# Performance work log

Measured on AMD Instinct MI355X. Metric: run time of the kernel, lower is better.

The kernel has to match this reference:

```python
import jax, jax.numpy as jnp
import numpy as np
from jax import lax

TIME_DIM = 100   # time_feat_dim
MEM_DIM = 172    # node_feat_dim == memory_dim
TAU = 0.3        # energy_threshold
LAM = 0.01       # softshrink sparsity_threshold


def _layer_norm(x, w, b, eps=1e-5):
    m = x.mean(-1, keepdims=True)
    v = ((x - m) ** 2).mean(-1, keepdims=True)
    return (x - m) / jnp.sqrt(v + eps) * w + b


def _time_encode(t):
    # TGN time encoder: cos(t * 1/10^linspace(0,9,D)), fixed (non-trainable)
    freqs = 1.0 / (10.0 ** jnp.linspace(0.0, 9.0, TIME_DIM))
    return jnp.cos(t[..., None] * freqs)


def _softshrink(x, lam=LAM):
    return jnp.where(x > lam, x - lam, jnp.where(x < -lam, x + lam, 0.0))


def setup_inputs() -> dict:
    key = jax.random.key(0)
    ks = jax.random.split(key, 12)
    B, N, NUM_NODES = 8192, 32, 500000
    s = 0.02  # scale used by Global_Local_Filtering
    return {
        "node_ids": jnp.arange(B, dtype=jnp.int32),
        "neighbor_node_ids": jax.random.randint(ks[0], (B, N), 0, NUM_NODES, dtype=jnp.int32),
        "node_interact_times": jax.random.uniform(ks[1], (B,), dtype=jnp.float32) * 1000.0,
        "neighbor_times": jax.random.uniform(ks[2], (B, N), dtype=jnp.float32) * 1000.0,
        "node_memories": jnp.zeros((NUM_NODES, MEM_DIM), jnp.float32),
        "r1": s * jax.random.normal(ks[3], (TIME_DIM, MEM_DIM), jnp.float32),
        "i1": s * jax.random.normal(ks[4], (TIME_DIM, MEM_DIM), jnp.float32),
        "rb1": s * jax.random.normal(ks[5], (MEM_DIM,), jnp.float32),
        "ib1": s * jax.random.normal(ks[6], (MEM_DIM,), jnp.float32),
        "conv_w": 0.02 * jax.random.normal(ks[7], (MEM_DIM, MEM_DIM, 8), jnp.float32),
        "conv_b": 0.02 * jax.random.normal(ks[8], (MEM_DIM,), jnp.float32),
        "rhythm_w": 0.1 * jax.random.normal(ks[9], (272, 1, 4), jnp.float32),
        "lin_w": 0.05 * jax.random.normal(ks[10], (272, MEM_DIM), jnp.float32),
        "lin_b": 0.02 * jax.random.normal(ks[11], (MEM_DIM,), jnp.float32),
        "mb_ln_w": jnp.ones((MEM_DIM,), jnp.float32),
        "mb_ln_b": jnp.zeros((MEM_DIM,), jnp.float32),
        "ln_w": jnp.ones((MEM_DIM,), jnp.float32),
        "ln_b": jnp.zeros((MEM_DIM,), jnp.float32),
    }


def reference(node_ids, neighbor_node_ids, node_interact_times, neighbor_times,
              node_memories, r1, i1, rb1, ib1, conv_w, conv_b,
              rhythm_w, lin_w, lin_b, mb_ln_w, mb_ln_b, ln_w, ln_b):
    # ---- RhythmMemoryUpdater.update_memory ----
    messages = _time_encode(node_interact_times)                 # [B,100]
    old_mem = node_memories[node_ids]                            # [B,172] gather
    x = jnp.concatenate([messages, old_mem], axis=-1)[:, :, None]  # [B,272,1] (NCH)
    # depthwise Conv1d(272,272,k=4,pad=2,groups=272,no bias): length 1 -> 2
    x = lax.conv_general_dilated(x, rhythm_w, (1,), [(2, 2)],
                                 dimension_numbers=("NCH", "OIH", "NCH"),
                                 feature_group_count=272)        # [B,272,2]
    x = jnp.einsum("bcl,cd->bld", x, lin_w) + lin_b              # [B,2,172]
    new_mem = x.mean(axis=1)                                     # mean(dim=1) since 2 != memory_dim
    # set_memories: layer_norm then scatter; then gather + SeqFilter layernorm
    updated = node_memories.at[node_ids].set(_layer_norm(new_mem, mb_ln_w, mb_ln_b))
    gathered = lax.stop_gradient(updated[node_ids])              # memory bank is non-trainable (no_grad)
    root_node_time = _layer_norm(gathered, ln_w, ln_b)           # [B,172]

    # ---- neighbor branch: FSTS (Global_Local_Filtering + Conv1d) ----
    dt = node_interact_times[:, None] - neighbor_times           # [B,N]
    tfeat = _time_encode(dt)                                     # [B,N,100]
    tfeat = jnp.where((neighbor_node_ids == 0)[..., None], 0.0, tfeat)

    xf = jnp.fft.fft(tfeat, axis=1, norm="ortho")                # [B,N,100] complex
    energy = jnp.sum(jnp.abs(xf) ** 2, axis=-1)                  # [B,N]
    mask = (energy / (energy.mean() + 1e-6) >= TAU).astype(tfeat.dtype)
    low = xf * mask[..., None]
    o_r = jnp.einsum("bnc,cd->bnd", low.real, r1) - jnp.einsum("bnc,cd->bnd", low.imag, i1) + rb1
    o_i = jnp.einsum("bnc,cd->bnd", low.imag, r1) + jnp.einsum("bnc,cd->bnd", low.real, i1) + ib1
    y_fft = _softshrink(jax.nn.relu(o_r)) + 1j * _softshrink(jax.nn.relu(o_i))
    y = jnp.fft.ifft(y_fft, axis=1, norm="ortho").real           # [B,N,172]

    # Local_Correlation: Conv1d(172,172,k=8,pad=4) over neighbor axis, then mean over length
    yc = lax.conv_general_dilated(y.transpose(0, 2, 1), conv_w, (1,), [(4, 4)],
                                  dimension_numbers=("NCH", "OIH", "NCH"))
    yc = yc + conv_b[None, :, None]                              # [B,172,33]
    neighbor_out = yc.mean(axis=-1)                              # [B,172]

    return root_node_time + neighbor_out
```

## Files before the change

### kernel.cpp

```cpp
#include <hip/hip_runtime.h>
#include <hip/hip_bf16.h>
#include <math.h>

#define B_ 8192
#define NN 32
#define TD 100
#define MD 172
#define KD 1376
#define TAUC 0.3f
#define LAMC 0.01f

typedef __attribute__((ext_vector_type(8))) short short8;
typedef __attribute__((ext_vector_type(4))) float f32x4;

#define WS_U_OFF    256
#define U_BYTES     ((size_t)B_ * KD * 2)
#define CONVB_ELEMS (11 * 43 * 64 * 8)
#define WBIG_ELEMS  (22 * 7 * 64 * 8)
#define CS_ELEMS    (2 * 64 * 8)
#define ROOT_ELEMS  (11 * 9 * 64 * 8)

__device__ __forceinline__ float wred(float v) {
#pragma unroll
  for (int o = 32; o > 0; o >>= 1) v += __shfl_down(v, o, 64);
  return v;
}

__device__ __forceinline__ short bf16_bits(float f) {
  __hip_bfloat16 h = __float2bfloat16(f);
  return *(short*)&h;
}

__device__ __forceinline__ unsigned pack2(float a, float b) {
  return (unsigned)(unsigned short)bf16_bits(a) |
         ((unsigned)(unsigned short)bf16_bits(b) << 16);
}

__global__ __launch_bounds__(256) void k_mean(const int* __restrict__ nid,
                                              const float* __restrict__ t,
                                              const float* __restrict__ nt,
                                              float* __restrict__ ws) {
  __shared__ float fr[TD];
  __shared__ float part[4];
  int tid = threadIdx.x;
  if (tid < TD) fr[tid] = (float)exp(-9.0 * (double)tid / 99.0 * 2.302585092994045684);
  __syncthreads();
  int idx = blockIdx.x * 256 + tid;
  int b = idx >> 5;
  float s = 0.f;
  if (nid[idx] != 0) {
    float dt = t[b] - nt[idx];
    for (int c = 0; c < TD; ++c) { float v = cosf(dt * fr[c]); s = fmaf(v, v, s); }
  }
  s = wred(s);
  if ((tid & 63) == 0) part[tid >> 6] = s;
  __syncthreads();
  if (tid == 0) atomicAdd(ws, part[0] + part[1] + part[2] + part[3]);
}

__global__ __launch_bounds__(256) void k_prep(const float* __restrict__ conv_w,
                                              short* __restrict__ Bfrag) {
  int idx = blockIdx.x * 256 + threadIdx.x;
  if (idx >= CONVB_ELEMS) return;
  int j = idx & 7;
  int l = (idx >> 3) & 63;
  int s = (idx >> 9) % 43;
  int n0 = idx / (43 * 64 * 8);
  int k = s * 32 + (l >> 4) * 8 + j;
  int col = n0 * 16 + (l & 15);
  float v = (col < MD) ? conv_w[(long)col * KD + k] : 0.f;
  Bfrag[idx] = bf16_bits(v);
}

__global__ __launch_bounds__(256) void k_prep3(const float* __restrict__ r1,
                                               const float* __restrict__ i1,
                                               const float* __restrict__ rhythm_w,
                                               const float* __restrict__ lin_w,
                                               short* __restrict__ Wfrag,
                                               short* __restrict__ CSfrag,
                                               short* __restrict__ Rfrag) {
  int idx = blockIdx.x * 256 + threadIdx.x;
  const float inv_s = 0.17677669529663687f;
  if (idx < WBIG_ELEMS) {
    int j = idx & 7;
    int l = (idx >> 3) & 63;
    int s = (idx % 3584) >> 9;
    int n0 = idx / 3584;
    int k = s * 32 + (l >> 4) * 8 + j;
    int col = n0 * 16 + (l & 15);
    float v = 0.f;
    if (k < 200) {
      if (n0 < 11) {
        int d = col;
        if (d < MD) v = (k < 100) ? r1[k * MD + d] : -i1[(k - 100) * MD + d];
      } else {
        int d = col - 176;
        if (d >= 0 && d < MD) v = (k < 100) ? i1[k * MD + d] : r1[(k - 100) * MD + d];
      }
    }
    Wfrag[idx] = bf16_bits(v);
  } else if (idx < WBIG_ELEMS + CS_ELEMS) {
    int idx2 = idx - WBIG_ELEMS;
    int j = idx2 & 7;
    int l = (idx2 >> 3) & 63;
    int s = idx2 >> 9;
    int row = l & 15;
    int kq = s * 32 + (l >> 4) * 8 + j;
    float v = 0.f;
    if (row < 8) {
      int kp = (kq < 32) ? kq : kq - 32;
      int lo = row - 4; if (lo < 0) lo = 0;
      int hi = row + 28; if (hi > 31) hi = 31;
      double cs = 0.0, ss = 0.0;
      for (int n = lo; n <= hi; ++n) {
        double ang = 0.19634954084936207740 * (double)((kp * n) & 31);
        cs += cos(ang); ss += sin(ang);
      }
      v = ((kq < 32) ? (float)cs : -(float)ss) * inv_s;
    }
    CSfrag[idx2] = bf16_bits(v);
  } else if (idx < WBIG_ELEMS + CS_ELEMS + ROOT_ELEMS) {
    int idx4 = idx - WBIG_ELEMS - CS_ELEMS;
    int n = idx4 / 4608;
    int rem = idx4 % 4608;
    int s = rem >> 9;
    int l = (rem >> 3) & 63;
    int j = rem & 7;
    int k = s * 32 + (l >> 4) * 8 + j;
    int col = n * 16 + (l & 15);
    float v = 0.f;
    if (k < 272 && col < MD) {
      float hw = 0.5f * (rhythm_w[k * 4 + 1] + rhythm_w[k * 4 + 2]);
      v = hw * lin_w[k * MD + col];
    }
    Rfrag[idx4] = bf16_bits(v);
  }
}

__global__ __launch_bounds__(384, 8) void k_main(
    const int* __restrict__ nbr_id, const float* __restrict__ t,
    const float* __restrict__ nt, const float* __restrict__ rb1,
    const float* __restrict__ ib1, const float* __restrict__ ws0,
    const short* __restrict__ Wfrag, const short* __restrict__ CSfrag,
    short* __restrict__ u_out) {
  __shared__ __align__(16) short sA[32 * 232];
  __shared__ __align__(16) unsigned char s_un[12800];
  __shared__ float s_fr[TD];
  __shared__ float s_c32[32], s_s32[32], s_dt[32], s_z[32];
  __shared__ float s_energy[32];

  float* tf = (float*)s_un;
  short* Y = (short*)s_un;
  const int tid = threadIdx.x;
  const int b = blockIdx.x;
  const int l = tid & 63, w = tid >> 6;
  const float inv_s = 0.17677669529663687f;

  if (tid < 32) {
    double ang = 0.19634954084936207740 * (double)tid;
    s_c32[tid] = (float)cos(ang);
    s_s32[tid] = (float)sin(ang);
    int gi = b * NN + tid;
    int id = nbr_id[gi];
    float d = t[b] - nt[gi];
    s_z[tid]  = (id == 0) ? 0.f : 1.f;
    s_dt[tid] = (id == 0) ? 0.f : d;
    s_energy[tid] = 0.f;
  }
  if (tid < TD) s_fr[tid] = (float)exp(-9.0 * (double)tid / 99.0 * 2.302585092994045684);
  __syncthreads();

  for (int idx = tid; idx < NN * TD; idx += 384) {
    int n = idx / TD, c = idx - n * TD;
    tf[idx] = s_z[n] * cosf(s_dt[n] * s_fr[c]);
  }
  if (tid < 256) {
    int row = tid >> 3, q = tid & 7;
    *(uint2*)(sA + row * 232 + 200 + q * 4) = make_uint2(0u, 0u);
  }
  __syncthreads();

  for (int task = tid; task < 17 * 25; task += 384) {
    int k = task / 25, c4 = (task - k * 25) * 4;
    float ar0=0,ar1=0,ar2=0,ar3=0, ai0=0,ai1=0,ai2=0,ai3=0;
    for (int n = 0; n < NN; ++n) {
      float4 a = *(const float4*)(tf + n * TD + c4);
      int j = (k * n) & 31;
      float cw = s_c32[j], sw = s_s32[j];
      ar0 = fmaf(a.x, cw, ar0); ai0 = fmaf(a.x, -sw, ai0);
      ar1 = fmaf(a.y, cw, ar1); ai1 = fmaf(a.y, -sw, ai1);
      ar2 = fmaf(a.z, cw, ar2); ai2 = fmaf(a.z, -sw, ai2);
      ar3 = fmaf(a.w, cw, ar3); ai3 = fmaf(a.w, -sw, ai3);
    }
    ar0*=inv_s; ar1*=inv_s; ar2*=inv_s; ar3*=inv_s;
    ai0*=inv_s; ai1*=inv_s; ai2*=inv_s; ai3*=inv_s;
    float e = ar0*ar0+ar1*ar1+ar2*ar2+ar3*ar3 + ai0*ai0+ai1*ai1+ai2*ai2+ai3*ai3;
    atomicAdd(&s_energy[k], e);
    uint2 vr = make_uint2(pack2(ar0, ar1), pack2(ar2, ar3));
    uint2 vi = make_uint2(pack2(ai0, ai1), pack2(ai2, ai3));
    *(uint2*)(sA + k * 232 + c4) = vr;
    *(uint2*)(sA + k * 232 + 100 + c4) = vi;
    if (k >= 1 && k <= 15) {
      uint2 vin = make_uint2(pack2(-ai0, -ai1), pack2(-ai2, -ai3));
      *(uint2*)(sA + (32 - k) * 232 + c4) = vr;
      *(uint2*)(sA + (32 - k) * 232 + 100 + c4) = vin;
    }
  }
  __syncthreads();

  {
    float gth = TAUC * (ws0[0] * (1.0f / 262144.0f) + 1e-6f);
    for (int idx = tid; idx < 800; idx += 384) {
      int row = idx / 25, q = idx - row * 25;
      int ks = (row <= 16) ? row : 32 - row;
      if (s_energy[ks] < gth)
        *(uint4*)((char*)sA + row * 464 + q * 16) = make_uint4(0u,0u,0u,0u);
    }
  }
  __syncthreads();

  const int mside = (w >= 3) ? 1 : 0;
  const int wn = w % 3;
  short8 afrag[7];
  {
    const short* ab = sA + (mside * 16 + (l & 15)) * 232 + ((l >> 4) << 3);
#pragma unroll
    for (int s = 0; s < 7; ++s) afrag[s] = *(const short8*)(ab + s * 32);
  }
  for (int n = wn; n < 11; n += 3) {
    f32x4 acc = (f32x4)(0.f);
#pragma unroll
    for (int s = 0; s < 7; ++s) {
      short8 bb = *(const short8*)(Wfrag + (((n * 7 + s) * 64) + l) * 8);
      acc = __builtin_amdgcn_mfma_f32_16x16x32_bf16(afrag[s], bb, acc, 0, 0, 0);
    }
    int d = n * 16 + (l & 15);
    bool valid = (d < MD);
    float bias = valid ? rb1[d] : 0.f;
    float y0 = valid ? fmaxf(acc[0] + bias - LAMC, 0.f) : 0.f;
    float y1 = valid ? fmaxf(acc[1] + bias - LAMC, 0.f) : 0.f;
    float y2 = valid ? fmaxf(acc[2] + bias - LAMC, 0.f) : 0.f;
    float y3 = valid ? fmaxf(acc[3] + bias - LAMC, 0.f) : 0.f;
    *(uint2*)(Y + d * 32 + mside * 16 + ((l >> 4) << 2)) =
        make_uint2(pack2(y0, y1), pack2(y2, y3));
  }
  __syncthreads();

  f32x4 uacc[2];
  uacc[0] = (f32x4)(0.f); uacc[1] = (f32x4)(0.f);
  {
    short8 cs0 = *(const short8*)(CSfrag + (l << 3));
#pragma unroll
    for (int ti = 0; ti < 2; ++ti) {
      int nu = w + 6 * ti;
      if (nu < 11) {
        short8 bfr = *(const short8*)(Y + (nu * 16 + (l & 15)) * 32 + ((l >> 4) << 3));
        uacc[ti] = __builtin_amdgcn_mfma_f32_16x16x32_bf16(cs0, bfr, uacc[ti], 0, 0, 0);
      }
    }
  }
  __syncthreads();

  for (int n = wn; n < 11; n += 3) {
    f32x4 acc = (f32x4)(0.f);
    int nw = n + 11;
#pragma unroll
    for (int s = 0; s < 7; ++s) {
      short8 bb = *(const short8*)(Wfrag + (((nw * 7 + s) * 64) + l) * 8);
      acc = __builtin_amdgcn_mfma_f32_16x16x32_bf16(afrag[s], bb, acc, 0, 0, 0);
    }
    int d = n * 16 + (l & 15);
    bool valid = (d < MD);
    float bias = valid ? ib1[d] : 0.f;
    float y0 = valid ? fmaxf(acc[0] + bias - LAMC, 0.f) : 0.f;
    float y1 = valid ? fmaxf(acc[1] + bias - LAMC, 0.f) : 0.f;
    float y2 = valid ? fmaxf(acc[2] + bias - LAMC, 0.f) : 0.f;
    float y3 = valid ? fmaxf(acc[3] + bias - LAMC, 0.f) : 0.f;
    *(uint2*)(Y + d * 32 + mside * 16 + ((l >> 4) << 2)) =
        make_uint2(pack2(y0, y1), pack2(y2, y3));
  }
  __syncthreads();

  {
    short8 cs1 = *(const short8*)(CSfrag + ((64 + l) << 3));
#pragma unroll
    for (int ti = 0; ti < 2; ++ti) {
      int nu = w + 6 * ti;
      if (nu < 11) {
        short8 bfr = *(const short8*)(Y + (nu * 16 + (l & 15)) * 32 + ((l >> 4) << 3));
        uacc[ti] = __builtin_amdgcn_mfma_f32_16x16x32_bf16(cs1, bfr, uacc[ti], 0, 0, 0);
        int q = l >> 4;
        int d = nu * 16 + (l & 15);
        if (q < 2 && d < MD) {
          uint2 pv = make_uint2(pack2(uacc[ti][0], uacc[ti][1]),
                                pack2(uacc[ti][2], uacc[ti][3]));
          *(uint2*)(u_out + (long)b * KD + d * 8 + q * 4) = pv;
        }
      }
    }
  }
}

__global__ __launch_bounds__(256) void k_tail(
    const int* __restrict__ node_ids, const float* __restrict__ t,
    const float* __restrict__ node_mem, const short* __restrict__ u,
    const short* __restrict__ convB, const float* __restrict__ conv_b,
    const short* __restrict__ Rfrag, const float* __restrict__ lin_b,
    const float* __restrict__ mb_w, const float* __restrict__ mb_b,
    const float* __restrict__ ln_w, const float* __restrict__ ln_b,
    float* __restrict__ out) {
  __shared__ __align__(16) unsigned char s_buf[11264];
  __shared__ float s_fq[TD];
  short* aR = (short*)s_buf;
  float* Ct = (float*)s_buf;
  const int tid = threadIdx.x;
  const int l = tid & 63, w = tid >> 6;
  const int b0 = blockIdx.x * 16;

  if (tid < TD) s_fq[tid] = (float)exp(-9.0 * (double)tid / 99.0 * 2.302585092994045684);
  __syncthreads();

  for (int idx = tid; idx < 16 * 296; idx += 256) {
    int r = idx / 296, c = idx - r * 296;
    float v = 0.f;
    if (c < TD) v = cosf(t[b0 + r] * s_fq[c]);
    else if (c < 272) v = node_mem[(long)node_ids[b0 + r] * MD + (c - TD)];
    aR[idx] = bf16_bits(v);
  }
  __syncthreads();

  const int start = w * 3;
  const int cnt = (w < 3) ? 3 : 2;
  f32x4 racc[3];
  racc[0] = (f32x4)(0.f); racc[1] = (f32x4)(0.f); racc[2] = (f32x4)(0.f);
  {
    const short* arp = aR + (l & 15) * 296 + ((l >> 4) << 3);
    for (int s = 0; s < 9; ++s) {
      short8 a = *(const short8*)(arp + s * 32);
#pragma unroll
      for (int tt = 0; tt < 3; ++tt) {
        if (tt < cnt) {
          int n = start + tt;
          short8 bb = *(const short8*)(Rfrag + (((n * 9 + s) * 64) + l) * 8);
          racc[tt] = __builtin_amdgcn_mfma_f32_16x16x32_bf16(a, bb, racc[tt], 0, 0, 0);
        }
      }
    }
  }
  f32x4 cacc[3];
  cacc[0] = (f32x4)(0.f); cacc[1] = (f32x4)(0.f); cacc[2] = (f32x4)(0.f);
  {
    const short* ap = u + (long)(b0 + (l & 15)) * KD + ((l >> 4) << 3);
    for (int s = 0; s < 43; ++s) {
      short8 a = *(const short8*)(ap + s * 32);
#pragma unroll
      for (int tt = 0; tt < 3; ++tt) {
        if (tt < cnt) {
          long n0 = start + tt;
          short8 bb = *(const short8*)(convB + ((n0 * 43 + s) * 64 + l) * 8);
          cacc[tt] = __builtin_amdgcn_mfma_f32_16x16x32_bf16(a, bb, cacc[tt], 0, 0, 0);
        }
      }
    }
  }
  __syncthreads();

#pragma unroll
  for (int tt = 0; tt < 3; ++tt) {
    if (tt < cnt) {
      int n = (start + tt) * 16 + (l & 15);
      if (n < MD) {
#pragma unroll
        for (int r = 0; r < 4; ++r)
          Ct[((l >> 4) * 4 + r) * 176 + n] = racc[tt][r];
      }
    }
  }
  __syncthreads();

  {
    int r = tid >> 4, g = tid & 15;
    float v[11];
    float sm = 0.f, sq = 0.f;
#pragma unroll
    for (int j = 0; j < 11; ++j) {
      int c = g + 16 * j;
      float x = (c < MD) ? (Ct[r * 176 + c] + lin_b[c]) : 0.f;
      v[j] = x; sm += x; sq += x * x;
    }
#pragma unroll
    for (int m = 1; m < 16; m <<= 1) { sm += __shfl_xor(sm, m, 64); sq += __shfl_xor(sq, m, 64); }
    float mean = sm / 172.f;
    float rstd = rsqrtf(sq / 172.f - mean * mean + 1e-5f);
    float sm2 = 0.f, sq2 = 0.f;
#pragma unroll
    for (int j = 0; j < 11; ++j) {
      int c = g + 16 * j;
      if (c < MD) {
        float h = (v[j] - mean) * rstd * mb_w[c] + mb_b[c];
        v[j] = h; sm2 += h; sq2 += h * h;
      }
    }
#pragma unroll
    for (int m = 1; m < 16; m <<= 1) { sm2 += __shfl_xor(sm2, m, 64); sq2 += __shfl_xor(sq2, m, 64); }
    float mean2 = sm2 / 172.f;
    float rstd2 = rsqrtf(sq2 / 172.f - mean2 * mean2 + 1e-5f);
#pragma unroll
    for (int j = 0; j < 11; ++j) {
      int c = g + 16 * j;
      if (c < MD) Ct[r * 176 + c] = (v[j] - mean2) * rstd2 * ln_w[c] + ln_b[c];
    }
  }
  __syncthreads();

#pragma unroll
  for (int tt = 0; tt < 3; ++tt) {
    if (tt < cnt) {
      int n = (start + tt) * 16 + (l & 15);
      if (n < MD) {
        float cb = conv_b[n];
#pragma unroll
        for (int r = 0; r < 4; ++r) {
          int mr = (l >> 4) * 4 + r;
          out[(long)(b0 + mr) * MD + n] =
              Ct[mr * 176 + n] + cacc[tt][r] * (1.0f / 33.0f) + cb;
        }
      }
    }
  }
}

extern "C" void kernel_launch(void* const* d_in, const int* in_sizes, int n_in,
                              void* d_out, int out_size, void* d_ws, size_t ws_size,
                              hipStream_t stream) {
  const int* node_ids = (const int*)d_in[0];
  const int* nbr_id   = (const int*)d_in[1];
  const float* t  = (const float*)d_in[2];
  const float* nt = (const float*)d_in[3];
  const float* node_mem = (const float*)d_in[4];
  const float* r1 = (const float*)d_in[5];
  const float* i1 = (const float*)d_in[6];
  const float* rb1 = (const float*)d_in[7];
  const float* ib1 = (const float*)d_in[8];
  const float* conv_w = (const float*)d_in[9];
  const float* conv_b = (const float*)d_in[10];
  const float* rhythm_w = (const float*)d_in[11];
  const float* lin_w = (const float*)d_in[12];
  const float* lin_b = (const float*)d_in[13];
  const float* mb_w = (const float*)d_in[14];
  const float* mb_b = (const float*)d_in[15];
  const float* ln_w = (const float*)d_in[16];
  const float* ln_b = (const float*)d_in[17];
  float* out = (float*)d_out;
  float* wsf = (float*)d_ws;

  char* base = (char*)d_ws;
  short* u      = (short*)(base + WS_U_OFF);
  short* convB  = (short*)(base + WS_U_OFF + U_BYTES);
  short* Wfrag  = convB + CONVB_ELEMS;
  short* CSfrag = Wfrag + WBIG_ELEMS;
  short* Rfrag  = CSfrag + CS_ELEMS;

  hipMemsetAsync(d_ws, 0, 16, stream);
  k_mean<<<1024, 256, 0, stream>>>(nbr_id, t, nt, wsf);
  k_prep<<<(CONVB_ELEMS + 255) / 256, 256, 0, stream>>>(conv_w, convB);
  k_prep3<<<(WBIG_ELEMS + CS_ELEMS + ROOT_ELEMS + 255) / 256, 256, 0, stream>>>(
      r1, i1, rhythm_w, lin_w, Wfrag, CSfrag, Rfrag);
  k_main<<<B_, 384, 0, stream>>>(nbr_id, t, nt, rb1, ib1, wsf, Wfrag, CSfrag, u);
  k_tail<<<512, 256, 0, stream>>>(node_ids, t, node_mem, u, convB, conv_b,
                                  Rfrag, lin_b, mb_w, mb_b, ln_w, ln_b, out);
}
```

Before: 652.2 us.

## Merge prep kernels, precompute trig tables, use fast cosine, rebalance tail waves

Combines the two weight-prep kernels into one launch that also writes a small table of frequencies and DFT twiddles, so the other kernels stop computing double-precision exp, cos and sin per block. Swaps cosf for a range-reduced hardware cosine intrinsic in the time-encoding loops. Grows the tail kernel to 512 threads so separate waves run the conv GEMM and the root GEMM in parallel instead of one after the other. The hardware cosine is less accurate, which matters for large arguments and could shift the energy mask near its threshold.

New measurement: 615.4 us. -5.6%, faster.

```diff
diff --git a/kernel.cpp b/kernel.cpp
--- a/kernel.cpp
+++ b/kernel.cpp
@@ -19,6 +19,8 @@
 #define WBIG_ELEMS  (22 * 7 * 64 * 8)
 #define CS_ELEMS    (2 * 64 * 8)
 #define ROOT_ELEMS  (11 * 9 * 64 * 8)
+#define FRAG_SHORTS (CONVB_ELEMS + WBIG_ELEMS + CS_ELEMS + ROOT_ELEMS)
+#define TBL_ELEMS   164
 
 __device__ __forceinline__ float wred(float v) {
 #pragma unroll
@@ -36,51 +38,32 @@
          ((unsigned)(unsigned short)bf16_bits(b) << 16);
 }
 
-__global__ __launch_bounds__(256) void k_mean(const int* __restrict__ nid,
-                                              const float* __restrict__ t,
-                                              const float* __restrict__ nt,
-                                              float* __restrict__ ws) {
-  __shared__ float fr[TD];
-  __shared__ float part[4];
-  int tid = threadIdx.x;
-  if (tid < TD) fr[tid] = (float)exp(-9.0 * (double)tid / 99.0 * 2.302585092994045684);
-  __syncthreads();
-  int idx = blockIdx.x * 256 + tid;
-  int b = idx >> 5;
-  float s = 0.f;
-  if (nid[idx] != 0) {
-    float dt = t[b] - nt[idx];
-    for (int c = 0; c < TD; ++c) { float v = cosf(dt * fr[c]); s = fmaf(v, v, s); }
-  }
-  s = wred(s);
-  if ((tid & 63) == 0) part[tid >> 6] = s;
-  __syncthreads();
-  if (tid == 0) atomicAdd(ws, part[0] + part[1] + part[2] + part[3]);
-}
-
-__global__ __launch_bounds__(256) void k_prep(const float* __restrict__ conv_w,
-                                              short* __restrict__ Bfrag) {
-  int idx = blockIdx.x * 256 + threadIdx.x;
-  if (idx >= CONVB_ELEMS) return;
-  int j = idx & 7;
-  int l = (idx >> 3) & 63;
-  int s = (idx >> 9) % 43;
-  int n0 = idx / (43 * 64 * 8);
-  int k = s * 32 + (l >> 4) * 8 + j;
-  int col = n0 * 16 + (l & 15);
-  float v = (col < MD) ? conv_w[(long)col * KD + k] : 0.f;
-  Bfrag[idx] = bf16_bits(v);
-}
-
-__global__ __launch_bounds__(256) void k_prep3(const float* __restrict__ r1,
-                                               const float* __restrict__ i1,
-                                               const float* __restrict__ rhythm_w,
-                                               const float* __restrict__ lin_w,
-                                               short* __restrict__ Wfrag,
-                                               short* __restrict__ CSfrag,
-                                               short* __restrict__ Rfrag) {
+__device__ __forceinline__ float fcos(float x) {
+  float r = x * 0.15915494309189535f;
+  r = r - floorf(r);
+  return __builtin_amdgcn_cosf(r);
+}
+
+__global__ __launch_bounds__(256) void k_prep0(
+    const float* __restrict__ conv_w, const float* __restrict__ r1,
+    const float* __restrict__ i1, const float* __restrict__ rhythm_w,
+    const float* __restrict__ lin_w, short* __restrict__ convB,
+    short* __restrict__ Wfrag, short* __restrict__ CSfrag,
+    short* __restrict__ Rfrag, float* __restrict__ tbl) {
   int idx = blockIdx.x * 256 + threadIdx.x;
   const float inv_s = 0.17677669529663687f;
+  if (idx < CONVB_ELEMS) {
+    int j = idx & 7;
+    int l = (idx >> 3) & 63;
+    int s = (idx >> 9) % 43;
+    int n0 = idx / (43 * 64 * 8);
+    int k = s * 32 + (l >> 4) * 8 + j;
+    int col = n0 * 16 + (l & 15);
+    float v = (col < MD) ? conv_w[(long)col * KD + k] : 0.f;
+    convB[idx] = bf16_bits(v);
+    return;
+  }
+  idx -= CONVB_ELEMS;
   if (idx < WBIG_ELEMS) {
     int j = idx & 7;
     int l = (idx >> 3) & 63;
@@ -99,11 +82,13 @@
       }
     }
     Wfrag[idx] = bf16_bits(v);
-  } else if (idx < WBIG_ELEMS + CS_ELEMS) {
-    int idx2 = idx - WBIG_ELEMS;
-    int j = idx2 & 7;
-    int l = (idx2 >> 3) & 63;
-    int s = idx2 >> 9;
+    return;
+  }
+  idx -= WBIG_ELEMS;
+  if (idx < CS_ELEMS) {
+    int j = idx & 7;
+    int l = (idx >> 3) & 63;
+    int s = idx >> 9;
     int row = l & 15;
     int kq = s * 32 + (l >> 4) * 8 + j;
     float v = 0.f;
@@ -118,11 +103,13 @@
       }
       v = ((kq < 32) ? (float)cs : -(float)ss) * inv_s;
     }
-    CSfrag[idx2] = bf16_bits(v);
-  } else if (idx < WBIG_ELEMS + CS_ELEMS + ROOT_ELEMS) {
-    int idx4 = idx - WBIG_ELEMS - CS_ELEMS;
-    int n = idx4 / 4608;
-    int rem = idx4 % 4608;
+    CSfrag[idx] = bf16_bits(v);
+    return;
+  }
+  idx -= CS_ELEMS;
+  if (idx < ROOT_ELEMS) {
+    int n = idx / 4608;
+    int rem = idx % 4608;
     int s = rem >> 9;
     int l = (rem >> 3) & 63;
     int j = rem & 7;
@@ -133,8 +120,40 @@
       float hw = 0.5f * (rhythm_w[k * 4 + 1] + rhythm_w[k * 4 + 2]);
       v = hw * lin_w[k * MD + col];
     }
-    Rfrag[idx4] = bf16_bits(v);
-  }
+    Rfrag[idx] = bf16_bits(v);
+    return;
+  }
+  idx -= ROOT_ELEMS;
+  if (idx < TBL_ELEMS) {
+    float v;
+    if (idx < 100)      v = (float)exp(-9.0 * (double)idx / 99.0 * 2.302585092994045684);
+    else if (idx < 132) v = (float)cos(0.19634954084936207740 * (double)(idx - 100));
+    else                v = (float)sin(0.19634954084936207740 * (double)(idx - 132));
+    tbl[idx] = v;
+  }
+}
+
+__global__ __launch_bounds__(256) void k_mean(const int* __restrict__ nid,
+                                              const float* __restrict__ t,
+                                              const float* __restrict__ nt,
+                                              const float* __restrict__ tbl,
+                                              float* __restrict__ ws) {
+  __shared__ float fr[TD];
+  __shared__ float part[4];
+  int tid = threadIdx.x;
+  if (tid < TD) fr[tid] = tbl[tid];
+  __syncthreads();
+  int idx = blockIdx.x * 256 + tid;
+  int b = idx >> 5;
+  float s = 0.f;
+  if (nid[idx] != 0) {
+    float dt = t[b] - nt[idx];
+    for (int c = 0; c < TD; ++c) { float v = fcos(dt * fr[c]); s = fmaf(v, v, s); }
+  }
+  s = wred(s);
+  if ((tid & 63) == 0) part[tid >> 6] = s;
+  __syncthreads();
+  if (tid == 0) atomicAdd(ws, part[0] + part[1] + part[2] + part[3]);
 }
 
 __global__ __launch_bounds__(384, 8) void k_main(
@@ -142,7 +161,7 @@
     const float* __restrict__ nt, const float* __restrict__ rb1,
     const float* __restrict__ ib1, const float* __restrict__ ws0,
     const short* __restrict__ Wfrag, const short* __restrict__ CSfrag,
-    short* __restrict__ u_out) {
+    const float* __restrict__ tbl, short* __restrict__ u_out) {
   __shared__ __align__(16) short sA[32 * 232];
   __shared__ __align__(16) unsigned char s_un[12800];
   __shared__ float s_fr[TD];
@@ -157,9 +176,8 @@
   const float inv_s = 0.17677669529663687f;
 
   if (tid < 32) {
-    double ang = 0.19634954084936207740 * (double)tid;
-    s_c32[tid] = (float)cos(ang);
-    s_s32[tid] = (float)sin(ang);
+    s_c32[tid] = tbl[100 + tid];
+    s_s32[tid] = tbl[132 + tid];
     int gi = b * NN + tid;
     int id = nbr_id[gi];
     float d = t[b] - nt[gi];
@@ -167,12 +185,12 @@
     s_dt[tid] = (id == 0) ? 0.f : d;
     s_energy[tid] = 0.f;
   }
-  if (tid < TD) s_fr[tid] = (float)exp(-9.0 * (double)tid / 99.0 * 2.302585092994045684);
+  if (tid < TD) s_fr[tid] = tbl[tid];
   __syncthreads();
 
   for (int idx = tid; idx < NN * TD; idx += 384) {
     int n = idx / TD, c = idx - n * TD;
-    tf[idx] = s_z[n] * cosf(s_dt[n] * s_fr[c]);
+    tf[idx] = s_z[n] * fcos(s_dt[n] * s_fr[c]);
   }
   if (tid < 256) {
     int row = tid >> 3, q = tid & 7;
@@ -301,84 +319,81 @@
   }
 }
 
-__global__ __launch_bounds__(256) void k_tail(
+__global__ __launch_bounds__(512) void k_tail(
     const int* __restrict__ node_ids, const float* __restrict__ t,
     const float* __restrict__ node_mem, const short* __restrict__ u,
     const short* __restrict__ convB, const float* __restrict__ conv_b,
     const short* __restrict__ Rfrag, const float* __restrict__ lin_b,
     const float* __restrict__ mb_w, const float* __restrict__ mb_b,
     const float* __restrict__ ln_w, const float* __restrict__ ln_b,
-    float* __restrict__ out) {
-  __shared__ __align__(16) unsigned char s_buf[11264];
-  __shared__ float s_fq[TD];
-  short* aR = (short*)s_buf;
-  float* Ct = (float*)s_buf;
+    const float* __restrict__ tbl, float* __restrict__ out) {
+  __shared__ __align__(16) short aR[16 * 296];
+  __shared__ __align__(16) float Ct[16 * 176];
   const int tid = threadIdx.x;
   const int l = tid & 63, w = tid >> 6;
   const int b0 = blockIdx.x * 16;
 
-  if (tid < TD) s_fq[tid] = (float)exp(-9.0 * (double)tid / 99.0 * 2.302585092994045684);
-  __syncthreads();
-
-  for (int idx = tid; idx < 16 * 296; idx += 256) {
+  for (int idx = tid; idx < 16 * 296; idx += 512) {
     int r = idx / 296, c = idx - r * 296;
     float v = 0.f;
-    if (c < TD) v = cosf(t[b0 + r] * s_fq[c]);
+    if (c < TD) v = fcos(t[b0 + r] * tbl[c]);
     else if (c < 272) v = node_mem[(long)node_ids[b0 + r] * MD + (c - TD)];
     aR[idx] = bf16_bits(v);
   }
   __syncthreads();
 
-  const int start = w * 3;
-  const int cnt = (w < 3) ? 3 : 2;
-  f32x4 racc[3];
-  racc[0] = (f32x4)(0.f); racc[1] = (f32x4)(0.f); racc[2] = (f32x4)(0.f);
-  {
+  const int cstart = (w < 5) ? w * 2 : 10;
+  const int ccnt = (w < 5) ? 2 : ((w == 5) ? 1 : 0);
+  f32x4 cacc[2];
+  cacc[0] = (f32x4)(0.f); cacc[1] = (f32x4)(0.f);
+  if (ccnt) {
+    const short* ap = u + (long)(b0 + (l & 15)) * KD + ((l >> 4) << 3);
+    for (int s = 0; s < 43; ++s) {
+      short8 a = *(const short8*)(ap + s * 32);
+#pragma unroll
+      for (int tt = 0; tt < 2; ++tt) {
+        if (tt < ccnt) {
+          long n0 = cstart + tt;
+          short8 bb = *(const short8*)(convB + ((n0 * 43 + s) * 64 + l) * 8);
+          cacc[tt] = __builtin_amdgcn_mfma_f32_16x16x32_bf16(a, bb, cacc[tt], 0, 0, 0);
+        }
+      }
+    }
+  }
+
+  const int rstart = (w == 5) ? 0 : ((w == 6) ? 3 : 7);
+  const int rcnt = (w == 5) ? 3 : ((w >= 6) ? 4 : 0);
+  if (rcnt) {
+    f32x4 racc[4];
+#pragma unroll
+    for (int tt = 0; tt < 4; ++tt) racc[tt] = (f32x4)(0.f);
     const short* arp = aR + (l & 15) * 296 + ((l >> 4) << 3);
     for (int s = 0; s < 9; ++s) {
       short8 a = *(const short8*)(arp + s * 32);
 #pragma unroll
-      for (int tt = 0; tt < 3; ++tt) {
-        if (tt < cnt) {
-          int n = start + tt;
+      for (int tt = 0; tt < 4; ++tt) {
+        if (tt < rcnt) {
+          int n = rstart + tt;
           short8 bb = *(const short8*)(Rfrag + (((n * 9 + s) * 64) + l) * 8);
           racc[tt] = __builtin_amdgcn_mfma_f32_16x16x32_bf16(a, bb, racc[tt], 0, 0, 0);
         }
       }
     }
-  }
-  f32x4 cacc[3];
-  cacc[0] = (f32x4)(0.f); cacc[1] = (f32x4)(0.f); cacc[2] = (f32x4)(0.f);
-  {
-    const short* ap = u + (long)(b0 + (l & 15)) * KD + ((l >> 4) << 3);
-    for (int s = 0; s < 43; ++s) {
-      short8 a = *(const short8*)(ap + s * 32);
-#pragma unroll
-      for (int tt = 0; tt < 3; ++tt) {
-        if (tt < cnt) {
-          long n0 = start + tt;
-          short8 bb = *(const short8*)(convB + ((n0 * 43 + s) * 64 + l) * 8);
-          cacc[tt] = __builtin_amdgcn_mfma_f32_16x16x32_bf16(a, bb, cacc[tt], 0, 0, 0);
+#pragma unroll
+    for (int tt = 0; tt < 4; ++tt) {
+      if (tt < rcnt) {
+        int n = (rstart + tt) * 16 + (l & 15);
+        if (n < MD) {
+#pragma unroll
+          for (int r = 0; r < 4; ++r)
+            Ct[((l >> 4) * 4 + r) * 176 + n] = racc[tt][r];
         }
       }
     }
   }
   __syncthreads();
 
-#pragma unroll
-  for (int tt = 0; tt < 3; ++tt) {
-    if (tt < cnt) {
-      int n = (start + tt) * 16 + (l & 15);
-      if (n < MD) {
-#pragma unroll
-        for (int r = 0; r < 4; ++r)
-          Ct[((l >> 4) * 4 + r) * 176 + n] = racc[tt][r];
-      }
-    }
-  }
-  __syncthreads();
-
-  {
+  if (tid < 256) {
     int r = tid >> 4, g = tid & 15;
     float v[11];
     float sm = 0.f, sq = 0.f;
@@ -414,9 +429,9 @@
   __syncthreads();
 
 #pragma unroll
-  for (int tt = 0; tt < 3; ++tt) {
-    if (tt < cnt) {
-      int n = (start + tt) * 16 + (l & 15);
+  for (int tt = 0; tt < 2; ++tt) {
+    if (tt < ccnt) {
+      int n = (cstart + tt) * 16 + (l & 15);
       if (n < MD) {
         float cb = conv_b[n];
 #pragma unroll
@@ -460,13 +475,13 @@
   short* Wfrag  = convB + CONVB_ELEMS;
   short* CSfrag = Wfrag + WBIG_ELEMS;
   short* Rfrag  = CSfrag + CS_ELEMS;
+  float* tbl    = (float*)(Rfrag + ROOT_ELEMS);
 
   hipMemsetAsync(d_ws, 0, 16, stream);
-  k_mean<<<1024, 256, 0, stream>>>(nbr_id, t, nt, wsf);
-  k_prep<<<(CONVB_ELEMS + 255) / 256, 256, 0, stream>>>(conv_w, convB);
-  k_prep3<<<(WBIG_ELEMS + CS_ELEMS + ROOT_ELEMS + 255) / 256, 256, 0, stream>>>(
-      r1, i1, rhythm_w, lin_w, Wfrag, CSfrag, Rfrag);
-  k_main<<<B_, 384, 0, stream>>>(nbr_id, t, nt, rb1, ib1, wsf, Wfrag, CSfrag, u);
-  k_tail<<<512, 256, 0, stream>>>(node_ids, t, node_mem, u, convB, conv_b,
-                                  Rfrag, lin_b, mb_w, mb_b, ln_w, ln_b, out);
-}
+  k_prep0<<<(FRAG_SHORTS + TBL_ELEMS + 255) / 256, 256, 0, stream>>>(
+      conv_w, r1, i1, rhythm_w, lin_w, convB, Wfrag, CSfrag, Rfrag, tbl);
+  k_mean<<<1024, 256, 0, stream>>>(nbr_id, t, nt, tbl, wsf);
+  k_main<<<B_, 384, 0, stream>>>(nbr_id, t, nt, rb1, ib1, wsf, Wfrag, CSfrag, tbl, u);
+  k_tail<<<512, 512, 0, stream>>>(node_ids, t, node_mem, u, convB, conv_b,
+                                  Rfrag, lin_b, mb_w, mb_b, ln_w, ln_b, tbl, out);
+}
```
